# Kernel optimization log

Hardware: AMD Instinct MI355X
Metric: run time of the kernel (lower is better)

The kernel has to match this reference:

```python
import jax, jax.numpy as jnp
import numpy as np

B, A, S, NC = 32, 3, 80, 80
EPS = 1e-7
LS = 0.1  # label smoothing


def setup_inputs() -> dict:
    key = jax.random.key(0)
    k1, k2, k3, k4, k5, k6 = jax.random.split(key, 6)
    pred = jax.random.normal(k1, (B, A, S, S, 5 + NC), dtype=jnp.float32)
    # structured target: obj flag in {0,1}, box cxcywh, class id (as float)
    obj = (jax.random.uniform(k2, (B, A, S, S)) < 0.05).astype(jnp.float32)
    xy = jax.random.uniform(k3, (B, A, S, S, 2))
    wh = jax.random.uniform(k4, (B, A, S, S, 2), minval=0.5, maxval=4.0)
    cls = jax.random.randint(k5, (B, A, S, S), 0, NC).astype(jnp.float32)
    target = jnp.concatenate([obj[..., None], xy, wh, cls[..., None]], axis=-1)
    anchors = jax.random.uniform(k6, (A, 2), minval=1.0, maxval=4.0)
    return {"pred": pred, "target": target, "anchors": anchors}


def _bce_logits(z, t):
    # numerically-stable BCEWithLogits: max(z,0) - z*t + log(1+exp(-|z|))
    return jnp.maximum(z, 0.0) - z * t + jnp.log1p(jnp.exp(-jnp.abs(z)))


def _masked_mean(x, m):
    return jnp.sum(x * m) / jnp.maximum(jnp.sum(m), 1.0)


def _ciou(b1, b2):
    # boxes [..., 4] in (cx, cy, w, h)
    cx1, cy1, w1, h1 = b1[..., 0], b1[..., 1], b1[..., 2], b1[..., 3]
    cx2, cy2, w2, h2 = b2[..., 0], b2[..., 1], b2[..., 2], b2[..., 3]
    x1a, x1b = cx1 - w1 * 0.5, cx1 + w1 * 0.5
    y1a, y1b = cy1 - h1 * 0.5, cy1 + h1 * 0.5
    x2a, x2b = cx2 - w2 * 0.5, cx2 + w2 * 0.5
    y2a, y2b = cy2 - h2 * 0.5, cy2 + h2 * 0.5
    iw = jnp.clip(jnp.minimum(x1b, x2b) - jnp.maximum(x1a, x2a), 0.0)
    ih = jnp.clip(jnp.minimum(y1b, y2b) - jnp.maximum(y1a, y2a), 0.0)
    inter = iw * ih
    union = w1 * h1 + w2 * h2 - inter + EPS
    iou = inter / union
    cw = jnp.maximum(x1b, x2b) - jnp.minimum(x1a, x2a)  # enclosing box
    ch = jnp.maximum(y1b, y2b) - jnp.minimum(y1a, y2a)
    c2 = cw * cw + ch * ch + EPS
    rho2 = (cx2 - cx1) ** 2 + (cy2 - cy1) ** 2
    four_over_pi2 = 4.0 / (np.pi ** 2)
    v = four_over_pi2 * (jnp.arctan(w2 / (h2 + EPS)) - jnp.arctan(w1 / (h1 + EPS))) ** 2
    alpha = v / (1.0 - iou + v + EPS)
    return iou - rho2 / c2 - alpha * v


def reference(pred, target, anchors):
    obj = (target[..., 0] == 1.0).astype(pred.dtype)    # [B,A,S,S]
    no_obj = (target[..., 0] == 0.0).astype(pred.dtype)
    # no-object BCE-with-logits on objectness channel (masked mean)
    no_object_loss = _masked_mean(_bce_logits(pred[..., 0], target[..., 0]), no_obj)
    # decoded box predictions: sigmoid xy, exp(wh)*anchors
    anc = anchors.reshape(1, A, 1, 1, 2)
    box_preds = jnp.concatenate(
        [jax.nn.sigmoid(pred[..., 1:3]), jnp.exp(pred[..., 3:5]) * anc], axis=-1)
    cious = _ciou(box_preds, target[..., 1:5])          # [B,A,S,S]
    box_loss = _masked_mean(1.0 - cious, obj)
    # note: original passes sigmoid(pred) INTO BCEWithLogits -> keep that quirk
    object_loss = _masked_mean(_bce_logits(jax.nn.sigmoid(pred[..., 0]), target[..., 0]), obj)
    # label-smoothed cross entropy on class logits
    logp = jax.nn.log_softmax(pred[..., 5:], axis=-1)   # [B,A,S,S,NC]
    cls_idx = target[..., 5].astype(jnp.int32)
    logp_y = jnp.take_along_axis(logp, cls_idx[..., None], axis=-1)[..., 0]
    ce = -((1.0 - LS) * logp_y + (LS / NC) * jnp.sum(logp, axis=-1))
    class_loss = _masked_mean(ce, obj)
    return 2.0 * box_loss + object_loss + no_object_loss + class_loss
```

## Files before the change

### kernel.cpp

```cpp
#include <hip/hip_runtime.h>
#include <cmath>

constexpr int Bn = 32, An = 3, Sn = 80, NCc = 80;
constexpr int NCELL = Bn * An * Sn * Sn;
constexpr int BDIM  = 256;
constexpr int NBLK  = NCELL / BDIM;
constexpr float EPSc = 1e-7f;

__device__ __forceinline__ float bce_logits(float z, float t) {
    return fmaxf(z, 0.f) - z * t + log1pf(expf(-fabsf(z)));
}

__global__ __launch_bounds__(BDIM) void yolo_main(
    const float* __restrict__ pred, const float* __restrict__ target,
    const float* __restrict__ anchors, float* __restrict__ partials)
{
    const int i    = blockIdx.x * BDIM + threadIdx.x;
    const int lane = threadIdx.x & 63;

    const float* tt = target + (size_t)i * 6;
    const float* pp = pred   + (size_t)i * 85;

    const float t0 = tt[0];
    const float z0 = pp[0];
    const bool obj   = (t0 == 1.0f);
    const bool noobj = (t0 == 0.0f);

    float nsum = 0.f, ncnt = 0.f, bsum = 0.f, osum = 0.f, csum = 0.f, ocnt = 0.f;

    if (noobj) {
        nsum = bce_logits(z0, t0);
        ncnt = 1.f;
    }

    if (obj) {
        const float p1 = pp[1], p2 = pp[2], p3 = pp[3], p4 = pp[4];
        const float px = 1.f / (1.f + expf(-p1));
        const float py = 1.f / (1.f + expf(-p2));
        const int   a  = (i / (Sn * Sn)) % An;
        const float pw = expf(p3) * anchors[2 * a];
        const float ph = expf(p4) * anchors[2 * a + 1];
        const float tx = tt[1], ty = tt[2], tw = tt[3], th = tt[4];

        const float x1a = px - pw * 0.5f, x1b = px + pw * 0.5f;
        const float y1a = py - ph * 0.5f, y1b = py + ph * 0.5f;
        const float x2a = tx - tw * 0.5f, x2b = tx + tw * 0.5f;
        const float y2a = ty - th * 0.5f, y2b = ty + th * 0.5f;

        const float iw = fmaxf(fminf(x1b, x2b) - fmaxf(x1a, x2a), 0.f);
        const float ih = fmaxf(fminf(y1b, y2b) - fmaxf(y1a, y2a), 0.f);
        const float inter = iw * ih;
        const float uni   = pw * ph + tw * th - inter + EPSc;
        const float iou   = inter / uni;

        const float cw = fmaxf(x1b, x2b) - fminf(x1a, x2a);
        const float ch = fmaxf(y1b, y2b) - fminf(y1a, y2a);
        const float c2 = cw * cw + ch * ch + EPSc;
        const float rho2 = (tx - px) * (tx - px) + (ty - py) * (ty - py);

        const float fopi2 = 4.0f / (3.14159265358979323846f * 3.14159265358979323846f);
        const float dv = atanf(tw / (th + EPSc)) - atanf(pw / (ph + EPSc));
        const float v  = fopi2 * dv * dv;
        const float alpha = v / (1.f - iou + v + EPSc);
        const float ciou  = iou - rho2 / c2 - alpha * v;

        bsum = 1.f - ciou;

        const float s0 = 1.f / (1.f + expf(-z0));
        osum = bce_logits(s0, t0);
        ocnt = 1.f;
    }

    unsigned long long mask = __ballot(obj);
    const int wave_base = i - lane;
    while (mask) {
        const int lj = __builtin_ctzll(mask);
        mask &= mask - 1;
        const int cj = wave_base + lj;

        const float* pc = pred + (size_t)cj * 85 + 5;
        const float z1 = pc[lane];
        const float z2 = (lane < NCc - 64) ? pc[64 + lane] : -INFINITY;

        float m = fmaxf(z1, z2);
        #pragma unroll
        for (int off = 32; off; off >>= 1) m = fmaxf(m, __shfl_xor(m, off));

        float e  = expf(z1 - m) + ((lane < NCc - 64) ? expf(z2 - m) : 0.f);
        float sz = z1 + ((lane < NCc - 64) ? z2 : 0.f);
        #pragma unroll
        for (int off = 32; off; off >>= 1) {
            e  += __shfl_xor(e, off);
            sz += __shfl_xor(sz, off);
        }
        const float lse = m + logf(e);

        const int k = (int)target[(size_t)cj * 6 + 5];
        const float zk = (k < 64) ? __shfl(z1, k) : __shfl(z2, k - 64);

        const float logp_y   = zk - lse;
        const float sum_logp = sz - (float)NCc * lse;
        const float ce = -(0.9f * logp_y + (0.1f / (float)NCc) * sum_logp);
        if (lane == 0) csum += ce;
    }

    #pragma unroll
    for (int off = 32; off; off >>= 1) {
        nsum += __shfl_xor(nsum, off);
        ncnt += __shfl_xor(ncnt, off);
        bsum += __shfl_xor(bsum, off);
        osum += __shfl_xor(osum, off);
        csum += __shfl_xor(csum, off);
        ocnt += __shfl_xor(ocnt, off);
    }

    __shared__ float red[4][6];
    const int w = threadIdx.x >> 6;
    if (lane == 0) {
        red[w][0] = nsum; red[w][1] = ncnt; red[w][2] = bsum;
        red[w][3] = osum; red[w][4] = csum; red[w][5] = ocnt;
    }
    __syncthreads();
    if (threadIdx.x < 6) {
        const int j = threadIdx.x;
        partials[(size_t)blockIdx.x * 8 + j] =
            red[0][j] + red[1][j] + red[2][j] + red[3][j];
    }
}

__global__ __launch_bounds__(256) void yolo_reduce(
    const float* __restrict__ partials, float* __restrict__ out)
{
    float s[6] = {0.f, 0.f, 0.f, 0.f, 0.f, 0.f};
    for (int b = threadIdx.x; b < NBLK; b += 256) {
        #pragma unroll
        for (int j = 0; j < 6; ++j) s[j] += partials[(size_t)b * 8 + j];
    }
    #pragma unroll
    for (int off = 32; off; off >>= 1) {
        #pragma unroll
        for (int j = 0; j < 6; ++j) s[j] += __shfl_xor(s[j], off);
    }
    __shared__ float red[4][6];
    const int w = threadIdx.x >> 6, lane = threadIdx.x & 63;
    if (lane == 0) {
        #pragma unroll
        for (int j = 0; j < 6; ++j) red[w][j] = s[j];
    }
    __syncthreads();
    if (threadIdx.x == 0) {
        float n[6];
        #pragma unroll
        for (int j = 0; j < 6; ++j)
            n[j] = red[0][j] + red[1][j] + red[2][j] + red[3][j];
        const float noobj_l = n[0] / fmaxf(n[1], 1.f);
        const float box_l   = n[2] / fmaxf(n[5], 1.f);
        const float obj_l   = n[3] / fmaxf(n[5], 1.f);
        const float cls_l   = n[4] / fmaxf(n[5], 1.f);
        out[0] = 2.f * box_l + obj_l + noobj_l + cls_l;
    }
}

extern "C" void kernel_launch(void* const* d_in, const int* in_sizes, int n_in,
                              void* d_out, int out_size, void* d_ws, size_t ws_size,
                              hipStream_t stream) {
    const float* pred    = (const float*)d_in[0];
    const float* target  = (const float*)d_in[1];
    const float* anchors = (const float*)d_in[2];
    float* out = (float*)d_out;
    float* partials = (float*)d_ws;

    yolo_main<<<NBLK, BDIM, 0, stream>>>(pred, target, anchors, partials);
    yolo_reduce<<<1, 256, 0, stream>>>(partials, out);
}
```

Baseline: 284.2 us.

## Use fast intrinsics, polynomial atan, paired class rows and derived no-obj count

Swaps exact expf/logf/divisions for __expf/__logf and hardware reciprocal, and replaces atanf with a minimax polynomial. The class cross-entropy loop now handles two object cells per iteration and drops the max subtraction, folding the label-smoothed terms into one reduction. It also reads the class id from the owning lane via shuffle instead of a global load, and infers the no-object count as total minus object count. This trims math and shuffle latency in a kernel that is mostly bandwidth-bound. The risks are lower accuracy, possible overflow in exp without max subtraction, and a count that is only correct when target flags are exactly 0 or 1.

```diff
diff --git a/kernel.cpp b/kernel.cpp
--- a/kernel.cpp
+++ b/kernel.cpp
@@ -7,8 +7,18 @@
 constexpr int NBLK  = NCELL / BDIM;
 constexpr float EPSc = 1e-7f;
 
-__device__ __forceinline__ float bce_logits(float z, float t) {
-    return fmaxf(z, 0.f) - z * t + log1pf(expf(-fabsf(z)));
+__device__ __forceinline__ float rcpf(float x) { return __builtin_amdgcn_rcpf(x); }
+
+__device__ __forceinline__ float fast_atan_pos(float x) {
+    const float inv = rcpf(x);
+    const float t  = fminf(x, inv);
+    const float t2 = t * t;
+    float p = fmaf(t2, 0.0208351f, -0.0851330f);
+    p = fmaf(t2, p, 0.1801410f);
+    p = fmaf(t2, p, -0.3302995f);
+    p = fmaf(t2, p, 0.9998660f);
+    const float a = t * p;
+    return (x > 1.f) ? (1.57079632679f - a) : a;
 }
 
 __global__ __launch_bounds__(BDIM) void yolo_main(
@@ -17,30 +27,31 @@
 {
     const int i    = blockIdx.x * BDIM + threadIdx.x;
     const int lane = threadIdx.x & 63;
+    const int wv   = threadIdx.x >> 6;
 
     const float* tt = target + (size_t)i * 6;
     const float* pp = pred   + (size_t)i * 85;
 
     const float t0 = tt[0];
     const float z0 = pp[0];
-    const bool obj   = (t0 == 1.0f);
-    const bool noobj = (t0 == 0.0f);
+    const bool obj = (t0 == 1.0f);
 
-    float nsum = 0.f, ncnt = 0.f, bsum = 0.f, osum = 0.f, csum = 0.f, ocnt = 0.f;
+    float nsum = 0.f, osum = 0.f, bsum = 0.f, ocnt = 0.f;
+    int   tk   = 0;
 
-    if (noobj) {
-        nsum = bce_logits(z0, t0);
-        ncnt = 1.f;
+    if (t0 == 0.0f) {
+        nsum = fmaxf(z0, 0.f) + __logf(1.f + __expf(-fabsf(z0)));
     }
 
     if (obj) {
         const float p1 = pp[1], p2 = pp[2], p3 = pp[3], p4 = pp[4];
-        const float px = 1.f / (1.f + expf(-p1));
-        const float py = 1.f / (1.f + expf(-p2));
+        const float px = rcpf(1.f + __expf(-p1));
+        const float py = rcpf(1.f + __expf(-p2));
         const int   a  = (i / (Sn * Sn)) % An;
-        const float pw = expf(p3) * anchors[2 * a];
-        const float ph = expf(p4) * anchors[2 * a + 1];
+        const float pw = __expf(p3) * anchors[2 * a];
+        const float ph = __expf(p4) * anchors[2 * a + 1];
         const float tx = tt[1], ty = tt[2], tw = tt[3], th = tt[4];
+        tk = (int)tt[5];
 
         const float x1a = px - pw * 0.5f, x1b = px + pw * 0.5f;
         const float y1a = py - ph * 0.5f, y1b = py + ph * 0.5f;
@@ -51,7 +62,7 @@
         const float ih = fmaxf(fminf(y1b, y2b) - fmaxf(y1a, y2a), 0.f);
         const float inter = iw * ih;
         const float uni   = pw * ph + tw * th - inter + EPSc;
-        const float iou   = inter / uni;
+        const float iou   = inter * rcpf(uni);
 
         const float cw = fmaxf(x1b, x2b) - fminf(x1a, x2a);
         const float ch = fmaxf(y1b, y2b) - fminf(y1a, y2a);
@@ -59,104 +70,112 @@
         const float rho2 = (tx - px) * (tx - px) + (ty - py) * (ty - py);
 
         const float fopi2 = 4.0f / (3.14159265358979323846f * 3.14159265358979323846f);
-        const float dv = atanf(tw / (th + EPSc)) - atanf(pw / (ph + EPSc));
+        const float dv = fast_atan_pos(tw * rcpf(th + EPSc))
+                       - fast_atan_pos(pw * rcpf(ph + EPSc));
         const float v  = fopi2 * dv * dv;
-        const float alpha = v / (1.f - iou + v + EPSc);
-        const float ciou  = iou - rho2 / c2 - alpha * v;
-
+        const float alpha = v * rcpf(1.f - iou + v + EPSc);
+        const float ciou  = iou - rho2 * rcpf(c2) - alpha * v;
         bsum = 1.f - ciou;
 
-        const float s0 = 1.f / (1.f + expf(-z0));
-        osum = bce_logits(s0, t0);
+        const float s = rcpf(1.f + __expf(-z0));
+        osum = __logf(1.f + __expf(-s));
         ocnt = 1.f;
     }
 
-    unsigned long long mask = __ballot(obj);
-    const int wave_base = i - lane;
-    while (mask) {
-        const int lj = __builtin_ctzll(mask);
-        mask &= mask - 1;
-        const int cj = wave_base + lj;
+    float csum = 0.f;
+    {
+        unsigned long long mask = __ballot(obj);
+        const int wbase = i - lane;
+        while (mask) {
+            const int lj0 = __builtin_ctzll(mask); mask &= mask - 1ull;
+            int lj1 = -1;
+            if (mask) { lj1 = __builtin_ctzll(mask); mask &= mask - 1ull; }
 
-        const float* pc = pred + (size_t)cj * 85 + 5;
-        const float z1 = pc[lane];
-        const float z2 = (lane < NCc - 64) ? pc[64 + lane] : -INFINITY;
+            const float* pa = pred + (size_t)(wbase + lj0) * 85 + 5;
+            const float* pb = (lj1 >= 0) ? (pred + (size_t)(wbase + lj1) * 85 + 5) : pa;
+            const float a1 = pa[lane];
+            const float a2 = (lane < 16) ? pa[64 + lane] : 0.f;
+            const float b1 = pb[lane];
+            const float b2 = (lane < 16) ? pb[64 + lane] : 0.f;
+            const int ka = __shfl(tk, lj0);
+            const int kb = (lj1 >= 0) ? __shfl(tk, lj1) : 0;
 
-        float m = fmaxf(z1, z2);
-        #pragma unroll
-        for (int off = 32; off; off >>= 1) m = fmaxf(m, __shfl_xor(m, off));
-
-        float e  = expf(z1 - m) + ((lane < NCc - 64) ? expf(z2 - m) : 0.f);
-        float sz = z1 + ((lane < NCc - 64) ? z2 : 0.f);
-        #pragma unroll
-        for (int off = 32; off; off >>= 1) {
-            e  += __shfl_xor(e, off);
-            sz += __shfl_xor(sz, off);
+            float ea = __expf(a1);
+            float ua = 0.00125f * a1 + ((lane == ka) ? 0.9f * a1 : 0.f);
+            float eb = __expf(b1);
+            float ub = 0.00125f * b1 + ((lane == kb) ? 0.9f * b1 : 0.f);
+            if (lane < 16) {
+                ea += __expf(a2);
+                ua += 0.00125f * a2 + ((64 + lane == ka) ? 0.9f * a2 : 0.f);
+                eb += __expf(b2);
+                ub += 0.00125f * b2 + ((64 + lane == kb) ? 0.9f * b2 : 0.f);
+            }
+            #pragma unroll
+            for (int off = 32; off; off >>= 1) {
+                ea += __shfl_xor(ea, off);
+                ua += __shfl_xor(ua, off);
+                eb += __shfl_xor(eb, off);
+                ub += __shfl_xor(ub, off);
+            }
+            float ce = __logf(ea) - ua;
+            if (lj1 >= 0) ce += __logf(eb) - ub;
+            if (lane == 0) csum += ce;
         }
-        const float lse = m + logf(e);
-
-        const int k = (int)target[(size_t)cj * 6 + 5];
-        const float zk = (k < 64) ? __shfl(z1, k) : __shfl(z2, k - 64);
-
-        const float logp_y   = zk - lse;
-        const float sum_logp = sz - (float)NCc * lse;
-        const float ce = -(0.9f * logp_y + (0.1f / (float)NCc) * sum_logp);
-        if (lane == 0) csum += ce;
     }
 
     #pragma unroll
     for (int off = 32; off; off >>= 1) {
         nsum += __shfl_xor(nsum, off);
-        ncnt += __shfl_xor(ncnt, off);
+        osum += __shfl_xor(osum, off);
         bsum += __shfl_xor(bsum, off);
-        osum += __shfl_xor(osum, off);
         csum += __shfl_xor(csum, off);
         ocnt += __shfl_xor(ocnt, off);
     }
 
-    __shared__ float red[4][6];
-    const int w = threadIdx.x >> 6;
+    __shared__ float red[4][5];
     if (lane == 0) {
-        red[w][0] = nsum; red[w][1] = ncnt; red[w][2] = bsum;
-        red[w][3] = osum; red[w][4] = csum; red[w][5] = ocnt;
+        red[wv][0] = nsum; red[wv][1] = osum; red[wv][2] = bsum;
+        red[wv][3] = csum; red[wv][4] = ocnt;
     }
     __syncthreads();
-    if (threadIdx.x < 6) {
+    if (threadIdx.x < 5) {
         const int j = threadIdx.x;
         partials[(size_t)blockIdx.x * 8 + j] =
             red[0][j] + red[1][j] + red[2][j] + red[3][j];
     }
 }
 
-__global__ __launch_bounds__(256) void yolo_reduce(
+__global__ __launch_bounds__(256) void yolo_finish(
     const float* __restrict__ partials, float* __restrict__ out)
 {
-    float s[6] = {0.f, 0.f, 0.f, 0.f, 0.f, 0.f};
+    float s[5] = {0.f, 0.f, 0.f, 0.f, 0.f};
     for (int b = threadIdx.x; b < NBLK; b += 256) {
         #pragma unroll
-        for (int j = 0; j < 6; ++j) s[j] += partials[(size_t)b * 8 + j];
+        for (int j = 0; j < 5; ++j) s[j] += partials[(size_t)b * 8 + j];
     }
     #pragma unroll
     for (int off = 32; off; off >>= 1) {
         #pragma unroll
-        for (int j = 0; j < 6; ++j) s[j] += __shfl_xor(s[j], off);
+        for (int j = 0; j < 5; ++j) s[j] += __shfl_xor(s[j], off);
     }
-    __shared__ float red[4][6];
-    const int w = threadIdx.x >> 6, lane = threadIdx.x & 63;
+    __shared__ float red[4][5];
+    const int wv = threadIdx.x >> 6, lane = threadIdx.x & 63;
     if (lane == 0) {
         #pragma unroll
-        for (int j = 0; j < 6; ++j) red[w][j] = s[j];
+        for (int j = 0; j < 5; ++j) red[wv][j] = s[j];
     }
     __syncthreads();
     if (threadIdx.x == 0) {
-        float n[6];
+        float n[5];
         #pragma unroll
-        for (int j = 0; j < 6; ++j)
+        for (int j = 0; j < 5; ++j)
             n[j] = red[0][j] + red[1][j] + red[2][j] + red[3][j];
-        const float noobj_l = n[0] / fmaxf(n[1], 1.f);
-        const float box_l   = n[2] / fmaxf(n[5], 1.f);
-        const float obj_l   = n[3] / fmaxf(n[5], 1.f);
-        const float cls_l   = n[4] / fmaxf(n[5], 1.f);
+        const float M  = n[4];
+        const float fM = fmaxf(M, 1.f);
+        const float noobj_l = n[0] / fmaxf((float)NCELL - M, 1.f);
+        const float obj_l   = n[1] / fM;
+        const float box_l   = n[2] / fM;
+        const float cls_l   = n[3] / fM;
         out[0] = 2.f * box_l + obj_l + noobj_l + cls_l;
     }
 }
@@ -171,5 +190,5 @@
     float* partials = (float*)d_ws;
 
     yolo_main<<<NBLK, BDIM, 0, stream>>>(pred, target, anchors, partials);
-    yolo_reduce<<<1, 256, 0, stream>>>(partials, out);
+    yolo_finish<<<1, 256, 0, stream>>>(partials, out);
 }
```

Result: faster. 274.9 us (-3.3%).
